# Optimization experiments

Measured on AMD Instinct MI355X. Metric: run time of the kernel, lower is better.

Reference implementation:

```python
import jax, jax.numpy as jnp
import numpy as np

B, T, I, H = 2048, 512, 9, 56


def _lstm_layer(x, w_ih, w_hh, b_ih, b_hh):
    """Single LSTM layer, batch_first x: [B, T, in] -> [B, T, H].
    PyTorch gate order: i, f, g, o."""
    # Precompute input projections for all timesteps in one GEMM: [B, T, 4H]
    xp = jnp.einsum('bti,gi->btg', x, w_ih) + b_ih + b_hh
    xp_t = jnp.transpose(xp, (1, 0, 2))  # [T, B, 4H]
    h0 = jnp.zeros((x.shape[0], w_hh.shape[1]), dtype=x.dtype)
    c0 = jnp.zeros_like(h0)

    def step(carry, xt):
        h, c = carry
        gates = xt + h @ w_hh.T  # [B, 4H]
        i, f, g, o = jnp.split(gates, 4, axis=-1)
        i = jax.nn.sigmoid(i)
        f = jax.nn.sigmoid(f)
        g = jnp.tanh(g)
        o = jax.nn.sigmoid(o)
        c = f * c + i * g
        h = o * jnp.tanh(c)
        return (h, c), h

    _, hs = jax.lax.scan(step, (h0, c0), xp_t)  # hs: [T, B, H]
    return jnp.transpose(hs, (1, 0, 2))  # [B, T, H]


def setup_inputs() -> dict:
    key = jax.random.key(0)
    ks = jax.random.split(key, 13)
    s_in = 1.0 / np.sqrt(H)
    inp = {
        'x': jax.random.normal(ks[0], (B, T, I), dtype=jnp.float32),
        'w_ih0': jax.random.uniform(ks[1], (4 * H, I), jnp.float32, -s_in, s_in),
        'w_hh0': jax.random.uniform(ks[2], (4 * H, H), jnp.float32, -s_in, s_in),
        'b_ih0': jax.random.uniform(ks[3], (4 * H,), jnp.float32, -s_in, s_in),
        'b_hh0': jax.random.uniform(ks[4], (4 * H,), jnp.float32, -s_in, s_in),
        'w_ih1': jax.random.uniform(ks[5], (4 * H, H), jnp.float32, -s_in, s_in),
        'w_hh1': jax.random.uniform(ks[6], (4 * H, H), jnp.float32, -s_in, s_in),
        'b_ih1': jax.random.uniform(ks[7], (4 * H,), jnp.float32, -s_in, s_in),
        'b_hh1': jax.random.uniform(ks[8], (4 * H,), jnp.float32, -s_in, s_in),
        'fc1_w': jax.random.uniform(ks[9], (H // 2, H), jnp.float32, -s_in, s_in),
        'fc1_b': jax.random.uniform(ks[10], (H // 2,), jnp.float32, -s_in, s_in),
        'fc2_w': jax.random.uniform(ks[11], (1, H // 2), jnp.float32, -0.2, 0.2),
        'fc2_b': jax.random.uniform(ks[12], (1,), jnp.float32, -0.2, 0.2),
    }
    return inp


def reference(x, w_ih0, w_hh0, b_ih0, b_hh0, w_ih1, w_hh1, b_ih1, b_hh1,
              fc1_w, fc1_b, fc2_w, fc2_b):
    h = _lstm_layer(x, w_ih0, w_hh0, b_ih0, b_hh0)   # [B, T, H]
    h = _lstm_layer(h, w_ih1, w_hh1, b_ih1, b_hh1)   # [B, T, H]
    last = h[:, -1]                                   # [B, H]
    y = jax.nn.relu(last @ fc1_w.T + fc1_b)           # [B, H//2]
    return y @ fc2_w.T + fc2_b                        # [B, 1]
```

## Files before the change

kernel.cpp:

```cpp
#include <hip/hip_runtime.h>
#include <stdint.h>

#define T_LEN 512
#define IN0   9
#define H     56
#define BG    8
#define NW    14
#define NTH   (NW * 64)
#define NBLK  256

typedef __attribute__((ext_vector_type(8))) short bfrag;
typedef __attribute__((ext_vector_type(4))) float ffrag;

#define MFMA(a,b,c) __builtin_amdgcn_mfma_f32_16x16x32_bf16((a),(b),(c),0,0,0)

__device__ __forceinline__ uint32_t bf16hi(float x) {
  uint32_t u = __float_as_uint(x);
  return (u + 0x7FFFu + ((u >> 16) & 1u)) & 0xFFFF0000u;
}
__device__ __forceinline__ void split_bf16(float x, short& hs, short& ls) {
  uint32_t hb = bf16hi(x);
  float lf = x - __uint_as_float(hb);
  hs = (short)(hb >> 16);
  ls = (short)(bf16hi(lf) >> 16);
}
__device__ __forceinline__ void split_bf16t(float x, short& hs, short& ls) {
  uint32_t hb = bf16hi(x);
  float lf = x - __uint_as_float(hb);
  hs = (short)(hb >> 16);
  ls = (short)(__float_as_uint(lf) >> 16);
}
__device__ __forceinline__ float dpp8(float v) {
  return __int_as_float(__builtin_amdgcn_update_dpp(0, __float_as_int(v), 0x128, 0xF, 0xF, true));
}
__device__ __forceinline__ float rcp_f(float v)  { return __builtin_amdgcn_rcpf(v); }
__device__ __forceinline__ float sigm_f(float v) { return rcp_f(1.0f + __expf(-v)); }
__device__ __forceinline__ float tanh_f(float v) { return 1.0f - 2.0f * rcp_f(1.0f + __expf(2.0f * v)); }

__device__ __forceinline__ int ftgt(int s) { return (s < 0) ? 0 : 7 * ((s >> 3) + 1); }

__device__ __forceinline__ void wait_flag(const int* f, int tgt) {
  if (tgt <= 0) return;
  const volatile int* vf = (const volatile int*)f;
  if (*vf < tgt) {
    int guard = 1 << 13;
    do { __builtin_amdgcn_s_sleep(2); } while (*vf < tgt && --guard);
  }
  asm volatile("" ::: "memory");
}

__global__ __launch_bounds__(NTH, 4)
void lstm_mfma13(const float* __restrict__ x,
                 const float* __restrict__ w_ih0, const float* __restrict__ w_hh0,
                 const float* __restrict__ b_ih0, const float* __restrict__ b_hh0,
                 const float* __restrict__ w_ih1, const float* __restrict__ w_hh1,
                 const float* __restrict__ b_ih1, const float* __restrict__ b_hh1,
                 const float* __restrict__ fc1_w, const float* __restrict__ fc1_b,
                 const float* __restrict__ fc2_w, const float* __restrict__ fc2_b,
                 float* __restrict__ out)
{
  __shared__ __align__(16) short hbufS[4 * 1024];
  __shared__ __align__(16) short xfS[T_LEN * 128];
  __shared__ __align__(16) float x8S[T_LEN * BG];
  __shared__ float sF[BG * H];
  __shared__ float sY[BG * 28];
  __shared__ int   flg[16];

  const int tid  = threadIdx.x;
  const int lane = tid & 63;
  const int w    = tid >> 6;
  const int c16  = lane & 15;
  const int quad = lane >> 4;

  const int  grp  = (w >= 7);
  const int  wg   = grp ? (w - 7) : w;
  const bool selB = (c16 >= 8);
  const int  b    = lane & 7;
  const int  sA   = 2 * wg, sB = 2 * wg + 1;
  const int  j_sel = 4 * (selB ? sB : sA) + quad;

  for (int i = tid; i < 2048; i += NTH) ((int*)hbufS)[i] = 0;
  if (tid < 16) flg[tid] = 0;

  const int kk   = j_sel & 31;
  const int offE = (j_sel >> 5) * 512 + ((kk >> 3) * 16 + b) * 8 + (kk & 7);

  for (int item = tid; item < T_LEN * BG; item += NTH) {
    const int t  = item & (T_LEN - 1);
    const int bb = item >> 9;
    const float* xr = x + ((size_t)(blockIdx.x * BG + bb) * T_LEN + t) * IN0;
    union { short s[8]; bfrag v; } hi, lo;
    #pragma unroll
    for (int q = 0; q < 8; ++q) split_bf16t(xr[q], hi.s[q], lo.s[q]);
    *(bfrag*)((char*)xfS + (size_t)t * 256 + bb * 16)       = hi.v;
    *(bfrag*)((char*)xfS + (size_t)t * 256 + (bb + 8) * 16) = lo.v;
    x8S[t * 8 + bb] = xr[8];
  }

  const char* const ldsb = (const char*)hbufS;
  const char* const xfb  = (const char*)xfS;
  const ffrag zerof = { 0.f, 0.f, 0.f, 0.f };
  const int incU1 = (quad == 3) ? 512 : 0;
  float cst = 0.f;

  __syncthreads();

#define SIGNAL(IDX8, STEP)                                                      \
  asm volatile("s_waitcnt lgkmcnt(0)" ::: "memory");                            \
  if (lane == 0) atomicAdd(&flg[(IDX8) + ((STEP) & 7)], 1);

  if (!grp) {
    bfrag B0hA[2], B0lA[2], B0hB[2], B0lB[2];
#define LOADW0(SUF, SIDX)                                                       \
    {                                                                           \
      const int np_ = 16 * (SIDX) + c16;                                        \
      const int wrow_ = (np_ & 3) * H + (np_ >> 2);                             \
      _Pragma("unroll")                                                         \
      for (int s = 0; s < 2; ++s) {                                             \
        union { short sh[8]; bfrag v; } ah, al;                                 \
        _Pragma("unroll")                                                       \
        for (int jj = 0; jj < 8; ++jj) {                                        \
          const int k = 32 * s + quad * 8 + jj;                                 \
          const float w0 = (k < H) ? w_hh0[wrow_ * H + k]                       \
                                   : w_ih0[wrow_ * IN0 + (k - 56)];             \
          split_bf16(w0, ah.sh[jj], al.sh[jj]);                                 \
        }                                                                       \
        B0h##SUF[s] = ah.v; B0l##SUF[s] = al.v;                                 \
      }                                                                         \
    }
    LOADW0(A, sA)
    LOADW0(B, sB)
#undef LOADW0

    ffrag bias0A, bias0B;
    #pragma unroll
    for (int r = 0; r < 4; ++r) {
      const int jA = 4 * sA + quad, jB = 4 * sB + quad;
      bias0A[r] = (c16 < 8) ? (b_ih0[r * H + jA] + b_hh0[r * H + jA]) : 0.0f;
      bias0B[r] = (c16 < 8) ? (b_ih0[r * H + jB] + b_hh0[r * H + jB]) : 0.0f;
    }
    float wx8s[4];
    #pragma unroll
    for (int r = 0; r < 4; ++r)
      wx8s[r] = w_ih0[(r * H + j_sel) * IN0 + 8];

    const char* const pU0_0 = ldsb + 2048 + lane * 16;
    const char* const pU0_1 = ldsb +        lane * 16;
    const char* pU1_0 = (quad == 3) ? (xfb +       c16 * 16) : (ldsb + 3072 + lane * 16);
    const char* pU1_1 = (quad == 3) ? (xfb + 256 + c16 * 16) : (ldsb + 1024 + lane * 16);
    const char* px8_0 = (const char*)x8S +      b * 4;
    const char* px8_1 = (const char*)x8S + 32 + b * 4;
    short* const hw_0 = hbufS +        offE;
    short* const hw_1 = hbufS + 1024 + offE;

#define STEP0(P, TT)                                                            \
    {                                                                           \
      const float x8v = *(const float*)px8_##P;                                 \
      wait_flag(&flg[((TT) - 1) & 7], ftgt((TT) - 1));                          \
      wait_flag(&flg[8 + (((TT) - 2) & 7)], ftgt((TT) - 2));                    \
      const bfrag U0 = *(const bfrag*)pU0_##P;                                  \
      const bfrag U1 = *(const bfrag*)pU1_##P;                                  \
      __builtin_amdgcn_s_setprio(1);                                            \
      ffrag aA = MFMA(B0hA[0], U0, bias0A);                                     \
      ffrag bA = MFMA(B0lA[0], U0, zerof);                                      \
      aA = MFMA(B0hA[1], U1, aA);                                               \
      bA = MFMA(B0lA[1], U1, bA);                                               \
      ffrag aB = MFMA(B0hB[0], U0, bias0B);                                     \
      ffrag bB = MFMA(B0lB[0], U0, zerof);                                      \
      aB = MFMA(B0hB[1], U1, aB);                                               \
      bB = MFMA(B0lB[1], U1, bB);                                               \
      __builtin_amdgcn_s_setprio(0);                                            \
      float sv[4];                                                              \
      _Pragma("unroll")                                                         \
      for (int r = 0; r < 4; ++r) {                                             \
        const float da = aA[r] + bA[r];                                         \
        const float db = aB[r] + bB[r];                                         \
        const float uu = selB ? db : da;                                        \
        const float vv = selB ? da : db;                                        \
        sv[r] = uu + dpp8(vv);                                                  \
      }                                                                         \
      const float gi = fmaf(wx8s[0], x8v, sv[0]);                               \
      const float gf = fmaf(wx8s[1], x8v, sv[1]);                               \
      const float gg = fmaf(wx8s[2], x8v, sv[2]);                               \
      const float go = fmaf(wx8s[3], x8v, sv[3]);                               \
      const float iv = sigm_f(gi), fv = sigm_f(gf);                             \
      const float gv = tanh_f(gg), ov = sigm_f(go);                             \
      cst = fmaf(fv, cst, iv * gv);                                             \
      const float hv = ov * tanh_f(cst);                                        \
      short hs, hl; split_bf16t(hv, hs, hl);                                    \
      hw_##P[0] = hs; hw_##P[64] = hl;                                          \
      SIGNAL(0, TT)                                                             \
    }

    for (int t = 0; t < T_LEN; t += 2) {
      STEP0(0, t)
      STEP0(1, t + 1)
      pU1_0 += incU1; pU1_1 += incU1;
      px8_0 += 64;    px8_1 += 64;
    }
#undef STEP0
  } else {
    bfrag BuhA[2], BhhA[2], BuhB[2], BhhB[2];
#define LOADW1(SUF, SIDX)                                                       \
    {                                                                           \
      const int np_ = 16 * (SIDX) + c16;                                        \
      const int wrow_ = (np_ & 3) * H + (np_ >> 2);                             \
      _Pragma("unroll")                                                         \
      for (int s = 0; s < 2; ++s) {                                             \
        union { short sh[8]; bfrag v; } au, ah;                                 \
        _Pragma("unroll")                                                       \
        for (int jj = 0; jj < 8; ++jj) {                                        \
          const int k = 32 * s + quad * 8 + jj;                                 \
          const float wu = (k < H) ? w_ih1[wrow_ * H + k] : 0.0f;               \
          const float wh = (k < H) ? w_hh1[wrow_ * H + k] : 0.0f;               \
          short dum;                                                            \
          split_bf16(wu, au.sh[jj], dum);                      \
          split_bf16(wh, ah.sh[jj], dum);                                       \
        }                                                                       \
        Buh##SUF[s] = au.v; Bhh##SUF[s] = ah.v;                                 \
      }                                                                         \
    }
    LOADW1(A, sA)
    LOADW1(B, sB)
#undef LOADW1

    ffrag bias1A, bias1B;
    #pragma unroll
    for (int r = 0; r < 4; ++r) {
      const int jA = 4 * sA + quad, jB = 4 * sB + quad;
      bias1A[r] = (c16 < 8) ? (b_ih1[r * H + jA] + b_hh1[r * H + jA]) : 0.0f;
      bias1B[r] = (c16 < 8) ? (b_ih1[r * H + jB] + b_hh1[r * H + jB]) : 0.0f;
    }

    const char* const qU0_0 = ldsb +        lane * 16;
    const char* const qU0_1 = ldsb + 2048 + lane * 16;
    const char* qU1_0 = (quad == 3) ? (xfb +       c16 * 16) : (ldsb + 1024 + lane * 16);
    const char* qU1_1 = (quad == 3) ? (xfb + 256 + c16 * 16) : (ldsb + 3072 + lane * 16);
    const char* const qH0_0 = ldsb + 4096 + 2048 + lane * 16;
    const char* const qH1_0 = qH0_0 + 1024;
    const char* const qH0_1 = ldsb + 4096 +        lane * 16;
    const char* const qH1_1 = qH0_1 + 1024;
    short* const qw_0 = hbufS + 2 * 1024 + offE;
    short* const qw_1 = hbufS + 3 * 1024 + offE;

#define STEP1(P, SS, LAST)                                                      \
    {                                                                           \
      wait_flag(&flg[(SS) & 7], ftgt(SS));                                      \
      wait_flag(&flg[8 + (((SS) - 1) & 7)], ftgt((SS) - 1));                    \
      const bfrag U0 = *(const bfrag*)qU0_##P;                                  \
      const bfrag U1 = *(const bfrag*)qU1_##P;                                  \
      const bfrag H0 = *(const bfrag*)qH0_##P;                                  \
      const bfrag H1 = *(const bfrag*)qH1_##P;                                  \
      __builtin_amdgcn_s_setprio(1);                                            \
      ffrag hA = MFMA(BhhA[0], H0, bias1A);                                     \
      hA = MFMA(BhhA[1], H1, hA);                                               \
      hA = MFMA(BuhA[0], U0, hA);                                               \
      hA = MFMA(BuhA[1], U1, hA);                                               \
      ffrag hBv = MFMA(BhhB[0], H0, bias1B);                                    \
      hBv = MFMA(BhhB[1], H1, hBv);                                             \
      hBv = MFMA(BuhB[0], U0, hBv);                                             \
      hBv = MFMA(BuhB[1], U1, hBv);                                             \
      __builtin_amdgcn_s_setprio(0);                                            \
      float sv[4];                                                              \
      _Pragma("unroll")                                                         \
      for (int r = 0; r < 4; ++r) {                                             \
        const float uu = selB ? hBv[r] : hA[r];                                 \
        const float vv = selB ? hA[r] : hBv[r];                                 \
        sv[r] = uu + dpp8(vv);                                                  \
      }                                                                         \
      const float iv = sigm_f(sv[0]), fv = sigm_f(sv[1]);                       \
      const float gv = tanh_f(sv[2]), ov = sigm_f(sv[3]);                       \
      cst = fmaf(fv, cst, iv * gv);                                             \
      const float hv = ov * tanh_f(cst);                                        \
      if (!(LAST)) {                                                            \
        short hs, hl; split_bf16t(hv, hs, hl);                                  \
        qw_##P[0] = hs; qw_##P[64] = hl;                                        \
        SIGNAL(8, SS)                                                           \
      } else {                                                                  \
        sF[b * H + j_sel] = hv;                                                 \
      }                                                                         \
    }

    for (int s = 0; s < T_LEN - 2; s += 2) {
      STEP1(0, s, 0)
      STEP1(1, s + 1, 0)
      qU1_0 += incU1; qU1_1 += incU1;
    }
    STEP1(0, T_LEN - 2, 0)
    STEP1(1, T_LEN - 1, 1)
#undef STEP1
  }
#undef SIGNAL

  __syncthreads();

  if (tid < 28 * BG) {
    const int m  = tid >> 3;
    const int bb = tid & 7;
    float acc = fc1_b[m];
    const float4* w4 = (const float4*)(fc1_w + m * H);
    const float4* h4 = (const float4*)(sF + bb * H);
    #pragma unroll
    for (int qq = 0; qq < H / 4; ++qq) {
      const float4 wv4 = w4[qq], hv4 = h4[qq];
      acc = fmaf(wv4.x, hv4.x, acc);
      acc = fmaf(wv4.y, hv4.y, acc);
      acc = fmaf(wv4.z, hv4.z, acc);
      acc = fmaf(wv4.w, hv4.w, acc);
    }
    sY[bb * 28 + m] = fmaxf(acc, 0.0f);
  }
  __syncthreads();
  if (tid < BG) {
    float acc = fc2_b[0];
    #pragma unroll
    for (int m = 0; m < 28; ++m)
      acc = fmaf(fc2_w[m], sY[tid * 28 + m], acc);
    out[blockIdx.x * BG + tid] = acc;
  }
}

extern "C" void kernel_launch(void* const* d_in, const int* in_sizes, int n_in,
                              void* d_out, int out_size, void* d_ws, size_t ws_size,
                              hipStream_t stream)
{
  const float* x     = (const float*)d_in[0];
  const float* w_ih0 = (const float*)d_in[1];
  const float* w_hh0 = (const float*)d_in[2];
  const float* b_ih0 = (const float*)d_in[3];
  const float* b_hh0 = (const float*)d_in[4];
  const float* w_ih1 = (const float*)d_in[5];
  const float* w_hh1 = (const float*)d_in[6];
  const float* b_ih1 = (const float*)d_in[7];
  const float* b_hh1 = (const float*)d_in[8];
  const float* fc1_w = (const float*)d_in[9];
  const float* fc1_b = (const float*)d_in[10];
  const float* fc2_w = (const float*)d_in[11];
  const float* fc2_b = (const float*)d_in[12];
  float* out = (float*)d_out;

  lstm_mfma13<<<NBLK, NTH, 0, stream>>>(
      x, w_ih0, w_hh0, b_ih0, b_hh0, w_ih1, w_hh1, b_ih1, b_hh1,
      fc1_w, fc1_b, fc2_w, fc2_b, out);
}
```

Baseline: 495.0 us.

## Quadruple-buffer layer-0 hidden state to decouple the two LSTM layer wave groups

Layer-0 hidden state now goes into four LDS buffers instead of two, so layer-0 waves only wait for layer 1 to have consumed step t-4 rather than t-2. That wait is moved to just before the store, after the MFMA and gate math. Flag reads are issued up front and the spin sleep is shortened, and both loops are unrolled by four. This should cut cross-group stalls between the producer and consumer layers, at the cost of more LDS and code size, which could affect occupancy.

New measurement: 479.3 us. 3.2% less time.

```diff
diff --git a/kernel.cpp b/kernel.cpp
--- a/kernel.cpp
+++ b/kernel.cpp
@@ -39,18 +39,17 @@
 
 __device__ __forceinline__ int ftgt(int s) { return (s < 0) ? 0 : 7 * ((s >> 3) + 1); }
 
-__device__ __forceinline__ void wait_flag(const int* f, int tgt) {
+__device__ __forceinline__ void wait_flag(const volatile int* vf, int tgt) {
   if (tgt <= 0) return;
-  const volatile int* vf = (const volatile int*)f;
   if (*vf < tgt) {
     int guard = 1 << 13;
-    do { __builtin_amdgcn_s_sleep(2); } while (*vf < tgt && --guard);
+    do { __builtin_amdgcn_s_sleep(1); } while (*vf < tgt && --guard);
   }
   asm volatile("" ::: "memory");
 }
 
 __global__ __launch_bounds__(NTH, 4)
-void lstm_mfma13(const float* __restrict__ x,
+void lstm_mfma14(const float* __restrict__ x,
                  const float* __restrict__ w_ih0, const float* __restrict__ w_hh0,
                  const float* __restrict__ b_ih0, const float* __restrict__ b_hh0,
                  const float* __restrict__ w_ih1, const float* __restrict__ w_hh1,
@@ -59,7 +58,7 @@
                  const float* __restrict__ fc2_w, const float* __restrict__ fc2_b,
                  float* __restrict__ out)
 {
-  __shared__ __align__(16) short hbufS[4 * 1024];
+  __shared__ __align__(16) short hbufS[6 * 1024];
   __shared__ __align__(16) short xfS[T_LEN * 128];
   __shared__ __align__(16) float x8S[T_LEN * BG];
   __shared__ float sF[BG * H];
@@ -79,7 +78,7 @@
   const int  sA   = 2 * wg, sB = 2 * wg + 1;
   const int  j_sel = 4 * (selB ? sB : sA) + quad;
 
-  for (int i = tid; i < 2048; i += NTH) ((int*)hbufS)[i] = 0;
+  for (int i = tid; i < 3072; i += NTH) ((int*)hbufS)[i] = 0;
   if (tid < 16) flg[tid] = 0;
 
   const int kk   = j_sel & 31;
@@ -100,7 +99,7 @@
   const char* const ldsb = (const char*)hbufS;
   const char* const xfb  = (const char*)xfS;
   const ffrag zerof = { 0.f, 0.f, 0.f, 0.f };
-  const int incU1 = (quad == 3) ? 512 : 0;
+  const int incU1 = (quad == 3) ? 1024 : 0;
   float cst = 0.f;
 
   __syncthreads();
@@ -144,20 +143,33 @@
     for (int r = 0; r < 4; ++r)
       wx8s[r] = w_ih0[(r * H + j_sel) * IN0 + 8];
 
-    const char* const pU0_0 = ldsb + 2048 + lane * 16;
-    const char* const pU0_1 = ldsb +        lane * 16;
-    const char* pU1_0 = (quad == 3) ? (xfb +       c16 * 16) : (ldsb + 3072 + lane * 16);
-    const char* pU1_1 = (quad == 3) ? (xfb + 256 + c16 * 16) : (ldsb + 1024 + lane * 16);
-    const char* px8_0 = (const char*)x8S +      b * 4;
-    const char* px8_1 = (const char*)x8S + 32 + b * 4;
-    short* const hw_0 = hbufS +        offE;
-    short* const hw_1 = hbufS + 1024 + offE;
+    const char* const pU0_0 = ldsb + 3 * 2048 + lane * 16;
+    const char* const pU0_1 = ldsb + 0 * 2048 + lane * 16;
+    const char* const pU0_2 = ldsb + 1 * 2048 + lane * 16;
+    const char* const pU0_3 = ldsb + 2 * 2048 + lane * 16;
+    const char* pU1_0 = (quad == 3) ? (xfb + 0 * 256 + c16 * 16) : (pU0_0 + 1024);
+    const char* pU1_1 = (quad == 3) ? (xfb + 1 * 256 + c16 * 16) : (pU0_1 + 1024);
+    const char* pU1_2 = (quad == 3) ? (xfb + 2 * 256 + c16 * 16) : (pU0_2 + 1024);
+    const char* pU1_3 = (quad == 3) ? (xfb + 3 * 256 + c16 * 16) : (pU0_3 + 1024);
+    const char* px8_0 = (const char*)x8S + 0 * 32 + b * 4;
+    const char* px8_1 = (const char*)x8S + 1 * 32 + b * 4;
+    const char* px8_2 = (const char*)x8S + 2 * 32 + b * 4;
+    const char* px8_3 = (const char*)x8S + 3 * 32 + b * 4;
+    short* const hw_0 = hbufS + 0 * 1024 + offE;
+    short* const hw_1 = hbufS + 1 * 1024 + offE;
+    short* const hw_2 = hbufS + 2 * 1024 + offE;
+    short* const hw_3 = hbufS + 3 * 1024 + offE;
 
 #define STEP0(P, TT)                                                            \
     {                                                                           \
       const float x8v = *(const float*)px8_##P;                                 \
-      wait_flag(&flg[((TT) - 1) & 7], ftgt((TT) - 1));                          \
-      wait_flag(&flg[8 + (((TT) - 2) & 7)], ftgt((TT) - 2));                    \
+      const volatile int* c0p_ = (const volatile int*)&flg[((TT) - 1) & 7];     \
+      const volatile int* c1p_ = (const volatile int*)&flg[8 + (((TT) - 4) & 7)]; \
+      const int v0_ = *c0p_;                     \
+      const int v1_ = *c1p_;                                                    \
+      const int t0_ = ftgt((TT) - 1), t1_ = ftgt((TT) - 4);                     \
+      if (v0_ < t0_) wait_flag(c0p_, t0_);                                      \
+      asm volatile("" ::: "memory");                                            \
       const bfrag U0 = *(const bfrag*)pU0_##P;                                  \
       const bfrag U1 = *(const bfrag*)pU1_##P;                                  \
       __builtin_amdgcn_s_setprio(1);                                            \
@@ -188,15 +200,19 @@
       cst = fmaf(fv, cst, iv * gv);                                             \
       const float hv = ov * tanh_f(cst);                                        \
       short hs, hl; split_bf16t(hv, hs, hl);                                    \
+      if (v1_ < t1_) wait_flag(c1p_, t1_);       \
+      asm volatile("" ::: "memory");                                            \
       hw_##P[0] = hs; hw_##P[64] = hl;                                          \
       SIGNAL(0, TT)                                                             \
     }
 
-    for (int t = 0; t < T_LEN; t += 2) {
+    for (int t = 0; t < T_LEN; t += 4) {
       STEP0(0, t)
       STEP0(1, t + 1)
-      pU1_0 += incU1; pU1_1 += incU1;
-      px8_0 += 64;    px8_1 += 64;
+      STEP0(2, t + 2)
+      STEP0(3, t + 3)
+      pU1_0 += incU1; pU1_1 += incU1; pU1_2 += incU1; pU1_3 += incU1;
+      px8_0 += 128;   px8_1 += 128;   px8_2 += 128;   px8_3 += 128;
     }
 #undef STEP0
   } else {
@@ -232,25 +248,37 @@
       bias1B[r] = (c16 < 8) ? (b_ih1[r * H + jB] + b_hh1[r * H + jB]) : 0.0f;
     }
 
-    const char* const qU0_0 = ldsb +        lane * 16;
-    const char* const qU0_1 = ldsb + 2048 + lane * 16;
-    const char* qU1_0 = (quad == 3) ? (xfb +       c16 * 16) : (ldsb + 1024 + lane * 16);
-    const char* qU1_1 = (quad == 3) ? (xfb + 256 + c16 * 16) : (ldsb + 3072 + lane * 16);
-    const char* const qH0_0 = ldsb + 4096 + 2048 + lane * 16;
-    const char* const qH1_0 = qH0_0 + 1024;
-    const char* const qH0_1 = ldsb + 4096 +        lane * 16;
-    const char* const qH1_1 = qH0_1 + 1024;
-    short* const qw_0 = hbufS + 2 * 1024 + offE;
-    short* const qw_1 = hbufS + 3 * 1024 + offE;
+    const char* const qU0_0 = ldsb + 0 * 2048 + lane * 16;
+    const char* const qU0_1 = ldsb + 1 * 2048 + lane * 16;
+    const char* const qU0_2 = ldsb + 2 * 2048 + lane * 16;
+    const char* const qU0_3 = ldsb + 3 * 2048 + lane * 16;
+    const char* qU1_0 = (quad == 3) ? (xfb + 0 * 256 + c16 * 16) : (qU0_0 + 1024);
+    const char* qU1_1 = (quad == 3) ? (xfb + 1 * 256 + c16 * 16) : (qU0_1 + 1024);
+    const char* qU1_2 = (quad == 3) ? (xfb + 2 * 256 + c16 * 16) : (qU0_2 + 1024);
+    const char* qU1_3 = (quad == 3) ? (xfb + 3 * 256 + c16 * 16) : (qU0_3 + 1024);
+    const char* const qH0_0 = ldsb + 8192 + 2048 + lane * 16;
+    const char* const qH0_1 = ldsb + 8192 +        lane * 16;
+    const char* const qH0_2 = qH0_0;
+    const char* const qH0_3 = qH0_1;
+    short* const qw_0 = hbufS + 4096 + 0 * 1024 + offE;
+    short* const qw_1 = hbufS + 4096 + 1 * 1024 + offE;
+    short* const qw_2 = qw_0;
+    short* const qw_3 = qw_1;
 
 #define STEP1(P, SS, LAST)                                                      \
     {                                                                           \
-      wait_flag(&flg[(SS) & 7], ftgt(SS));                                      \
-      wait_flag(&flg[8 + (((SS) - 1) & 7)], ftgt((SS) - 1));                    \
+      const volatile int* f0_ = (const volatile int*)&flg[(SS) & 7];            \
+      const volatile int* f1_ = (const volatile int*)&flg[8 + (((SS) - 1) & 7)]; \
+      const int v0_ = *f0_;                      \
+      const int v1_ = *f1_;                                                     \
+      const int t0_ = ftgt(SS), t1_ = ftgt((SS) - 1);                           \
+      if (v0_ < t0_) wait_flag(f0_, t0_);                                       \
+      if (v1_ < t1_) wait_flag(f1_, t1_);                                       \
+      asm volatile("" ::: "memory");                                            \
       const bfrag U0 = *(const bfrag*)qU0_##P;                                  \
       const bfrag U1 = *(const bfrag*)qU1_##P;                                  \
       const bfrag H0 = *(const bfrag*)qH0_##P;                                  \
-      const bfrag H1 = *(const bfrag*)qH1_##P;                                  \
+      const bfrag H1 = *(const bfrag*)(qH0_##P + 1024);                         \
       __builtin_amdgcn_s_setprio(1);                                            \
       ffrag hA = MFMA(BhhA[0], H0, bias1A);                                     \
       hA = MFMA(BhhA[1], H1, hA);                                               \
@@ -281,13 +309,17 @@
       }                                                                         \
     }
 
-    for (int s = 0; s < T_LEN - 2; s += 2) {
+    for (int s = 0; s < T_LEN - 4; s += 4) {
       STEP1(0, s, 0)
       STEP1(1, s + 1, 0)
-      qU1_0 += incU1; qU1_1 += incU1;
-    }
-    STEP1(0, T_LEN - 2, 0)
-    STEP1(1, T_LEN - 1, 1)
+      STEP1(2, s + 2, 0)
+      STEP1(3, s + 3, 0)
+      qU1_0 += incU1; qU1_1 += incU1; qU1_2 += incU1; qU1_3 += incU1;
+    }
+    STEP1(0, T_LEN - 4, 0)
+    STEP1(1, T_LEN - 3, 0)
+    STEP1(2, T_LEN - 2, 0)
+    STEP1(3, T_LEN - 1, 1)
 #undef STEP1
   }
 #undef SIGNAL
@@ -339,7 +371,7 @@
   const float* fc2_b = (const float*)d_in[12];
   float* out = (float*)d_out;
 
-  lstm_mfma13<<<NBLK, NTH, 0, stream>>>(
+  lstm_mfma14<<<NBLK, NTH, 0, stream>>>(
       x, w_ih0, w_hh0, b_ih0, b_hh0, w_ih1, w_hh1, b_ih1, b_hh1,
       fc1_w, fc1_b, fc2_w, fc2_b, out);
 }
```
